# Kernel optimization log

Measured on AMD Instinct MI355X. Metric: run time of the kernel, lower is better.

The kernel has to match this reference:

```python
import jax, jax.numpy as jnp
import numpy as np

N, E, D, D_OUT = 100000, 3200000, 64, 64
EPS = 1e-5


def setup_inputs() -> dict:
    key = jax.random.key(0)
    ks = jax.random.split(key, 16)
    s = 1.0 / np.sqrt(D)
    inp = {
        "x": jax.random.normal(ks[0], (N, D), dtype=jnp.float32),
        "edge_index": jax.random.randint(ks[1], (2, E), 0, N, dtype=jnp.int64),
        # layer 1: GCNConv weight/bias, fc weight/bias, BN gamma/beta
        "W1": jax.random.uniform(ks[2], (D, D), jnp.float32, -s, s),
        "b1": jnp.zeros((D,), jnp.float32),
        "fw1": jax.random.uniform(ks[3], (D, D), jnp.float32, -s, s),
        "fb1": jax.random.uniform(ks[4], (D,), jnp.float32, -s, s),
        "g1": jnp.ones((D,), jnp.float32),
        "bt1": jnp.zeros((D,), jnp.float32),
        # layer 2
        "W2": jax.random.uniform(ks[5], (D, D), jnp.float32, -s, s),
        "b2": jnp.zeros((D,), jnp.float32),
        "fw2": jax.random.uniform(ks[6], (D, D_OUT), jnp.float32, -s, s),
        "fb2": jax.random.uniform(ks[7], (D_OUT,), jnp.float32, -s, s),
        "g2": jnp.ones((D_OUT,), jnp.float32),
        "bt2": jnp.zeros((D_OUT,), jnp.float32),
    }
    return inp


def _gcn_conv(x, W, b, src, dst, dinv):
    # x' = X W, then symmetric-normalized scatter-add aggregation (self loops included)
    h = x @ W                                   # [N, D]
    msg = (dinv[src] * dinv[dst])[:, None] * h[src]  # [E+N, D]
    out = jax.ops.segment_sum(msg, dst, num_segments=N)
    return out + b


def _fc_bn_relu(x, fw, fb, g, bt):
    y = x @ fw + fb
    mu = jnp.mean(y, axis=0)
    var = jnp.mean((y - mu) ** 2, axis=0)  # biased var (torch BN training mode)
    y = (y - mu) * jax.lax.rsqrt(var + EPS) * g + bt
    return jax.nn.relu(y)


def reference(x, edge_index, W1, b1, fw1, fb1, g1, bt1, W2, b2, fw2, fb2, g2, bt2):
    loop = jnp.arange(N, dtype=edge_index.dtype)
    src = jnp.concatenate([edge_index[0], loop])  # add self loops
    dst = jnp.concatenate([edge_index[1], loop])
    deg = jax.ops.segment_sum(jnp.ones_like(dst, dtype=x.dtype), dst, num_segments=N)
    dinv = jax.lax.rsqrt(deg)  # deg >= 1 thanks to self loops

    h = _gcn_conv(x, W1, b1, src, dst, dinv)
    h = _fc_bn_relu(h, fw1, fb1, g1, bt1)
    h = _gcn_conv(h, W2, b2, src, dst, dinv)
    h = _fc_bn_relu(h, fw2, fb2, g2, bt2)
    return h
```

## Files before the change

### kernel.cpp

```cpp
#include <hip/hip_runtime.h>

#define N_NODES 100000
#define N_EDGES 3200000
#define D 64
#define EPS 1e-5f

#define BSHIFT 7
#define BNODES 128
#define NBUCK ((N_NODES + BNODES - 1) / BNODES)
#define P1_CHUNK 4096
#define NB_P1 ((N_EDGES + P1_CHUNK - 1) / P1_CHUNK)
#define SRC_MASK 0x1FFFFu
#define BCAP 4480
#define TBL_STRIDE 784

typedef _Float16 f16x8 __attribute__((ext_vector_type(8)));
typedef _Float16 half2v __attribute__((ext_vector_type(2)));
typedef unsigned int u32x4 __attribute__((ext_vector_type(4)));
typedef __attribute__((ext_vector_type(4))) float f32x4;

__device__ __forceinline__ unsigned short f2h(float f) {
  return __builtin_bit_cast(unsigned short, (_Float16)f);
}
__device__ __forceinline__ half2v u2h(unsigned int u) {
  return __builtin_bit_cast(half2v, u);
}
__device__ __forceinline__ unsigned int h2u(half2v h) {
  return __builtin_bit_cast(unsigned int, h);
}
__device__ __forceinline__ float2 hpair(unsigned int u) {
  half2v h = __builtin_bit_cast(half2v, u);
  return make_float2((float)h.x, (float)h.y);
}
__device__ __forceinline__ void addp(half2v a[4], uint4 u) {
  a[0] += u2h(u.x);
  a[1] += u2h(u.y);
  a[2] += u2h(u.z);
  a[3] += u2h(u.w);
}

__global__ __launch_bounds__(256) void combine_weights(
    const float* __restrict__ W1, const float* __restrict__ b1,
    const float* __restrict__ fw1, const float* __restrict__ fb1,
    const float* __restrict__ W2, const float* __restrict__ b2,
    const float* __restrict__ fw2, const float* __restrict__ fb2,
    unsigned int* __restrict__ WcB1, float* __restrict__ bc1,
    unsigned int* __restrict__ WcB2, float* __restrict__ bc2,
    float* __restrict__ stats) {
  if (blockIdx.x == 2) {
    if (threadIdx.x < 256) stats[threadIdx.x] = 0.0f;
    return;
  }
  const float* W  = blockIdx.x ? W2  : W1;
  const float* fw = blockIdx.x ? fw2 : fw1;
  const float* b  = blockIdx.x ? b2  : b1;
  const float* fb = blockIdx.x ? fb2 : fb1;
  unsigned int* WcB = blockIdx.x ? WcB2 : WcB1;
  float* bc = blockIdx.x ? bc2 : bc1;

  __shared__ float sW[64 * 64];
  __shared__ float sf[64 * 64];
  __shared__ float sC[64 * 64];
  for (int i = threadIdx.x; i < 4096; i += 256) { sW[i] = W[i]; sf[i] = fw[i]; }
  __syncthreads();
  for (int o = threadIdx.x; o < 4096; o += 256) {
    int i = o >> 6, j = o & 63;
    float acc = 0.f;
    #pragma unroll
    for (int k = 0; k < 64; ++k) acc += sW[i * 64 + k] * sf[k * 64 + j];
    sC[o] = acc;
  }
  __syncthreads();
  for (int o = threadIdx.x; o < 2048; o += 256) {
    int jj = o & 3, L = (o >> 2) & 63, kh = (o >> 8) & 1, nt = o >> 9;
    int k0 = (L >> 4) * 8 + jj * 2 + kh * 32;
    int n  = nt * 16 + (L & 15);
    unsigned int lo = f2h(sC[k0 * 64 + n]);
    unsigned int hi = f2h(sC[(k0 + 1) * 64 + n]);
    WcB[o] = (hi << 16) | lo;
  }
  if (threadIdx.x < 64) {
    int j = threadIdx.x;
    float acc = fb[j];
    #pragma unroll
    for (int k = 0; k < 64; ++k) acc += b[k] * sf[k * 64 + j];
    bc[j] = acc;
  }
}

__global__ __launch_bounds__(256) void pass1_sort(
    const int* __restrict__ src, const int* __restrict__ dst,
    unsigned int* __restrict__ stage, unsigned short* __restrict__ tbl) {
  __shared__ unsigned int hist[NBUCK];
  __shared__ unsigned int ts[256];
  __shared__ unsigned int sorted[P1_CHUNK];
  const int tid = threadIdx.x;
  const int e0 = blockIdx.x * P1_CHUNK;

  for (int b = tid; b < NBUCK; b += 256) hist[b] = 0;
  __syncthreads();

  int dreg[16];
  #pragma unroll
  for (int k = 0; k < 16; ++k) {
    int e = e0 + k * 256 + tid;
    int d = (e < N_EDGES) ? dst[e] : -1;
    dreg[k] = d;
    if (d >= 0) atomicAdd(&hist[((unsigned)d) >> BSHIFT], 1u);
  }
  __syncthreads();

  unsigned int v[4], run = 0;
  #pragma unroll
  for (int j = 0; j < 4; ++j) {
    int bk = 4 * tid + j;
    unsigned int h = (bk < NBUCK) ? hist[bk] : 0u;
    v[j] = run;
    run += h;
  }
  ts[tid] = run;
  __syncthreads();
  for (int o = 1; o < 256; o <<= 1) {
    unsigned int add = (tid >= o) ? ts[tid - o] : 0u;
    __syncthreads();
    ts[tid] += add;
    __syncthreads();
  }
  const unsigned int excl = ts[tid] - run;
  const unsigned int m = ts[255];
  unsigned short* trow = tbl + (size_t)blockIdx.x * TBL_STRIDE;
  #pragma unroll
  for (int j = 0; j < 4; ++j) {
    int bk = 4 * tid + j;
    if (bk < NBUCK) {
      unsigned int o = excl + v[j];
      hist[bk] = o;
      trow[bk] = (unsigned short)o;
    }
  }
  if (tid == 0) trow[NBUCK] = (unsigned short)m;
  __syncthreads();

  #pragma unroll
  for (int k = 0; k < 16; ++k) {
    int e = e0 + k * 256 + tid;
    int t = dreg[k];
    if (t >= 0) {
      unsigned int pos = atomicAdd(&hist[((unsigned)t) >> BSHIFT], 1u);
      sorted[pos] = (((unsigned)(t & (BNODES - 1))) << 17) | (unsigned)src[e];
    }
  }
  __syncthreads();

  unsigned int* so = stage + (size_t)blockIdx.x * P1_CHUNK;
  for (int i = tid; i < (int)m; i += 256) so[i] = sorted[i];
}

__global__ __launch_bounds__(512) void pass2_sort(
    const unsigned int* __restrict__ stage, const unsigned short* __restrict__ tbl,
    int* __restrict__ eSrc, int* __restrict__ off, int* __restrict__ edeg,
    float* __restrict__ dinv, const float* __restrict__ x,
    unsigned short* __restrict__ Xs) {
  __shared__ int spre[512];
  __shared__ int cnt[BNODES];
  __shared__ int ts[BNODES];
  __shared__ float dinvL[BNODES];
  __shared__ unsigned int raw[BCAP];
  __shared__ int sorted[BCAP];
  const int b = blockIdx.x, tid = threadIdx.x;
  const int n0 = b * BNODES;

  int base0 = 0, base1 = 0, len0 = 0, len1 = 0;
  {
    int s0 = 2 * tid, s1 = 2 * tid + 1;
    if (s0 < NB_P1) {
      const unsigned short* trow = tbl + (size_t)s0 * TBL_STRIDE;
      int o0 = trow[b], o1 = trow[b + 1];
      base0 = s0 * P1_CHUNK + o0;
      len0 = o1 - o0;
    }
    if (s1 < NB_P1) {
      const unsigned short* trow = tbl + (size_t)s1 * TBL_STRIDE;
      int o0 = trow[b], o1 = trow[b + 1];
      base1 = s1 * P1_CHUNK + o0;
      len1 = o1 - o0;
    }
  }
  if (tid < BNODES) cnt[tid] = 0;
  const int mylen = len0 + len1;
  spre[tid] = mylen;
  __syncthreads();
  for (int o = 1; o < 512; o <<= 1) {
    int add = (tid >= o) ? spre[tid - o] : 0;
    __syncthreads();
    spre[tid] += add;
    __syncthreads();
  }
  const int m = spre[511];
  const int pref = spre[tid] - mylen;

  for (int j = 0; j < len0; ++j) {
    unsigned int p = stage[base0 + j];
    raw[pref + j] = p;
    atomicAdd(&cnt[p >> 17], 1);
  }
  for (int j = 0; j < len1; ++j) {
    unsigned int p = stage[base1 + j];
    raw[pref + len0 + j] = p;
    atomicAdd(&cnt[p >> 17], 1);
  }
  __syncthreads();

  int v = 0;
  if (tid < BNODES) { v = cnt[tid]; ts[tid] = v; }
  __syncthreads();
  for (int o = 1; o < BNODES; o <<= 1) {
    int add = (tid >= o && tid < BNODES) ? ts[tid - o] : 0;
    __syncthreads();
    if (tid < BNODES) ts[tid] += add;
    __syncthreads();
  }
  if (tid < BNODES) {
    int excl = ts[tid] - v;
    int node = n0 + tid;
    float dv = rsqrtf((float)v + 1.0f);
    dinvL[tid] = dv;
    if (node < N_NODES) {
      off[node]  = b * BCAP + excl;
      edeg[node] = v;
      dinv[node] = dv;
    }
    cnt[tid] = excl;
  }
  __syncthreads();

  for (int i = tid; i < m; i += 512) {
    unsigned int p = raw[i];
    int pos = atomicAdd(&cnt[p >> 17], 1);
    if (pos < BCAP) sorted[pos] = (int)(p & SRC_MASK);
  }
  __syncthreads();

  int* out = eSrc + (size_t)b * BCAP;
  for (int i = tid; i < m; i += 512) out[i] = sorted[i];

  const int rows = min(BNODES, N_NODES - n0);
  for (int i = tid; i < rows * 64; i += 512) {
    int r = i >> 6;
    size_t g = (size_t)(n0 + r) * 64 + (i & 63);
    Xs[g] = f2h(dinvL[r] * x[g]);
  }
}

__global__ __launch_bounds__(256) void agg_csr(
    const int* __restrict__ off, const int* __restrict__ edeg,
    const int* __restrict__ eSrc, const unsigned short* __restrict__ Xs,
    const float* __restrict__ dinv, unsigned short* __restrict__ agg) {
  const int wv = (blockIdx.x * 256 + threadIdx.x) >> 6;
  const int lane = threadIdx.x & 63;
  const int half = lane >> 5;
  const int l32 = lane & 31;
  const int grp = l32 >> 3;
  const int sub = lane & 7;
  const int node = wv * 2 + half;
  if (node >= N_NODES) return;

  const int s0 = off[node];
  const int deg = edeg[node];
  const float dvf = dinv[node];
  const uint4* XsV = (const uint4*)Xs;

  int eidx = node;
  if (deg > 0) {
    int li = (l32 < deg) ? l32 : deg - 1;
    eidx = __builtin_nontemporal_load(&eSrc[s0 + li]);
  }

  half2v acc[4];
  {
    uint4 u = XsV[(size_t)node * 8 + sub];
    if (l32 >= 8) { u.x = 0; u.y = 0; u.z = 0; u.w = 0; }
    acc[0] = u2h(u.x);
    acc[1] = u2h(u.y);
    acc[2] = u2h(u.z);
    acc[3] = u2h(u.w);
  }

  uint4 g[8];
  #pragma unroll
  for (int j = 0; j < 8; ++j) {
    int srcn = __shfl(eidx, half * 32 + j * 4 + grp, 64);
    g[j] = XsV[(size_t)srcn * 8 + sub];
  }
  #pragma unroll
  for (int j = 0; j < 8; ++j) {
    uint4 u = g[j];
    if (j * 4 + grp >= deg) { u.x = 0; u.y = 0; u.z = 0; u.w = 0; }
    addp(acc, u);
  }

  if (deg > 32) {
    const int lim = deg - 1;
    for (int e = 32; e < deg; e += 4) {
      int ee = e + grp;
      int srcn = __builtin_nontemporal_load(&eSrc[s0 + min(ee, lim)]);
      uint4 u = XsV[(size_t)srcn * 8 + sub];
      if (ee > lim) { u.x = 0; u.y = 0; u.z = 0; u.w = 0; }
      addp(acc, u);
    }
  }

  #pragma unroll
  for (int mk = 8; mk <= 16; mk <<= 1) {
    #pragma unroll
    for (int i = 0; i < 4; ++i)
      acc[i] += u2h(__shfl_xor(h2u(acc[i]), mk, 64));
  }

  if (l32 < 8) {
    _Float16 dh = (_Float16)dvf;
    half2v d2 = {dh, dh};
    u32x4 o;
    o.x = h2u(acc[0] * d2);
    o.y = h2u(acc[1] * d2);
    o.z = h2u(acc[2] * d2);
    o.w = h2u(acc[3] * d2);
    __builtin_nontemporal_store(o, (u32x4*)(agg + (size_t)node * 64 + sub * 8));
  }
}

__global__ __launch_bounds__(256) void gemm_stats(
    const unsigned short* __restrict__ A, const unsigned int* __restrict__ WcB,
    const float* __restrict__ bc, unsigned short* __restrict__ Yb,
    float* __restrict__ colsum, float* __restrict__ colsq) {
  const int tid = threadIdx.x;
  const int L = tid & 63, wv = tid >> 6;
  const int quad = L >> 4, l16 = L & 15;

  const f16x8* Wv = (const f16x8*)WcB;
  f16x8 bfr[4][2];
  #pragma unroll
  for (int nt = 0; nt < 4; ++nt)
    #pragma unroll
    for (int kh = 0; kh < 2; ++kh)
      bfr[nt][kh] = Wv[(nt * 2 + kh) * 64 + L];
  float bcv[4];
  #pragma unroll
  for (int nt = 0; nt < 4; ++nt) bcv[nt] = bc[nt * 16 + l16];

  const f16x8* Av = (const f16x8*)A;
  float psum[4] = {0.f, 0.f, 0.f, 0.f}, psq[4] = {0.f, 0.f, 0.f, 0.f};

  #pragma unroll
  for (int loop = 0; loop < 2; ++loop) {
    const int rowbase = blockIdx.x * 128 + loop * 64 + wv * 16;
    const int m = min(rowbase + l16, N_NODES - 1);
    f16x8 a0 = Av[(size_t)m * 8 + quad];
    f16x8 a1 = Av[(size_t)m * 8 + 4 + quad];
    #pragma unroll
    for (int nt = 0; nt < 4; ++nt) {
      f32x4 acc = {0.f, 0.f, 0.f, 0.f};
      acc = __builtin_amdgcn_mfma_f32_16x16x32_f16(a0, bfr[nt][0], acc, 0, 0, 0);
      acc = __builtin_amdgcn_mfma_f32_16x16x32_f16(a1, bfr[nt][1], acc, 0, 0, 0);
      #pragma unroll
      for (int r = 0; r < 4; ++r) {
        int row = rowbase + quad * 4 + r;
        if (row < N_NODES) {
          float y = acc[r] + bcv[nt];
          Yb[(size_t)row * 64 + nt * 16 + l16] = f2h(y);
          psum[nt] += y;
          psq[nt] += y * y;
        }
      }
    }
  }

  #pragma unroll
  for (int nt = 0; nt < 4; ++nt) {
    psum[nt] += __shfl_xor(psum[nt], 16, 64);
    psum[nt] += __shfl_xor(psum[nt], 32, 64);
    psq[nt]  += __shfl_xor(psq[nt], 16, 64);
    psq[nt]  += __shfl_xor(psq[nt], 32, 64);
  }
  __shared__ float rsum[4][64];
  __shared__ float rsq[4][64];
  if (L < 16) {
    #pragma unroll
    for (int nt = 0; nt < 4; ++nt) {
      rsum[wv][nt * 16 + L] = psum[nt];
      rsq[wv][nt * 16 + L]  = psq[nt];
    }
  }
  __syncthreads();
  if (tid < 64) {
    float s = rsum[0][tid] + rsum[1][tid] + rsum[2][tid] + rsum[3][tid];
    float q = rsq[0][tid] + rsq[1][tid] + rsq[2][tid] + rsq[3][tid];
    atomicAdd(&colsum[tid], s);
    atomicAdd(&colsq[tid], q);
  }
}

__global__ __launch_bounds__(256) void prescale_y(
    unsigned short* __restrict__ YbXs, const float* __restrict__ dinv,
    const float* __restrict__ colsum, const float* __restrict__ colsq,
    const float* __restrict__ g, const float* __restrict__ bt) {
  __shared__ float sa[64], sc[64];
  if (threadIdx.x < 64) {
    int j = threadIdx.x;
    float mu = colsum[j] * (1.0f / N_NODES);
    float var = colsq[j] * (1.0f / N_NODES) - mu * mu;
    float s = rsqrtf(var + EPS) * g[j];
    sa[j] = s;
    sc[j] = bt[j] - mu * s;
  }
  __syncthreads();
  int idx = blockIdx.x * blockDim.x + threadIdx.x;
  if (idx < N_NODES * 8) {
    int r = idx >> 3, c0 = (idx & 7) * 8;
    float dv = dinv[r];
    uint4 u = ((const uint4*)YbXs)[idx];
    float2 p0 = hpair(u.x), p1 = hpair(u.y), p2 = hpair(u.z), p3 = hpair(u.w);
    p0.x = dv * fmaxf(fmaf(p0.x, sa[c0    ], sc[c0    ]), 0.f);
    p0.y = dv * fmaxf(fmaf(p0.y, sa[c0 + 1], sc[c0 + 1]), 0.f);
    p1.x = dv * fmaxf(fmaf(p1.x, sa[c0 + 2], sc[c0 + 2]), 0.f);
    p1.y = dv * fmaxf(fmaf(p1.y, sa[c0 + 3], sc[c0 + 3]), 0.f);
    p2.x = dv * fmaxf(fmaf(p2.x, sa[c0 + 4], sc[c0 + 4]), 0.f);
    p2.y = dv * fmaxf(fmaf(p2.y, sa[c0 + 5], sc[c0 + 5]), 0.f);
    p3.x = dv * fmaxf(fmaf(p3.x, sa[c0 + 6], sc[c0 + 6]), 0.f);
    p3.y = dv * fmaxf(fmaf(p3.y, sa[c0 + 7], sc[c0 + 7]), 0.f);
    uint4 o;
    o.x = ((unsigned)f2h(p0.y) << 16) | f2h(p0.x);
    o.y = ((unsigned)f2h(p1.y) << 16) | f2h(p1.x);
    o.z = ((unsigned)f2h(p2.y) << 16) | f2h(p2.x);
    o.w = ((unsigned)f2h(p3.y) << 16) | f2h(p3.x);
    ((uint4*)YbXs)[idx] = o;
  }
}

__global__ __launch_bounds__(256) void final_norm(
    const unsigned short* __restrict__ Yb, float* __restrict__ out,
    const float* __restrict__ colsum, const float* __restrict__ colsq,
    const float* __restrict__ g, const float* __restrict__ bt) {
  __shared__ float sa[64], sc[64];
  if (threadIdx.x < 64) {
    int j = threadIdx.x;
    float mu = colsum[j] * (1.0f / N_NODES);
    float var = colsq[j] * (1.0f / N_NODES) - mu * mu;
    float s = rsqrtf(var + EPS) * g[j];
    sa[j] = s;
    sc[j] = bt[j] - mu * s;
  }
  __syncthreads();
  int idx = blockIdx.x * blockDim.x + threadIdx.x;
  if (idx < N_NODES * 8) {
    int c0 = (idx & 7) * 8;
    uint4 u = ((const uint4*)Yb)[idx];
    float2 p0 = hpair(u.x), p1 = hpair(u.y), p2 = hpair(u.z), p3 = hpair(u.w);
    float4 o0, o1;
    o0.x = fmaxf(fmaf(p0.x, sa[c0    ], sc[c0    ]), 0.f);
    o0.y = fmaxf(fmaf(p0.y, sa[c0 + 1], sc[c0 + 1]), 0.f);
    o0.z = fmaxf(fmaf(p1.x, sa[c0 + 2], sc[c0 + 2]), 0.f);
    o0.w = fmaxf(fmaf(p1.y, sa[c0 + 3], sc[c0 + 3]), 0.f);
    o1.x = fmaxf(fmaf(p2.x, sa[c0 + 4], sc[c0 + 4]), 0.f);
    o1.y = fmaxf(fmaf(p2.y, sa[c0 + 5], sc[c0 + 5]), 0.f);
    o1.z = fmaxf(fmaf(p3.x, sa[c0 + 6], sc[c0 + 6]), 0.f);
    o1.w = fmaxf(fmaf(p3.y, sa[c0 + 7], sc[c0 + 7]), 0.f);
    ((float4*)out)[idx * 2] = o0;
    ((float4*)out)[idx * 2 + 1] = o1;
  }
}

extern "C" void kernel_launch(void* const* d_in, const int* in_sizes, int n_in,
                              void* d_out, int out_size, void* d_ws, size_t ws_size,
                              hipStream_t stream) {
  const float* x   = (const float*)d_in[0];
  const int*   src = (const int*)d_in[1];
  const int*   dst = src + N_EDGES;
  const float* W1  = (const float*)d_in[2];
  const float* b1  = (const float*)d_in[3];
  const float* fw1 = (const float*)d_in[4];
  const float* fb1 = (const float*)d_in[5];
  const float* g1  = (const float*)d_in[6];
  const float* bt1 = (const float*)d_in[7];
  const float* W2  = (const float*)d_in[8];
  const float* b2  = (const float*)d_in[9];
  const float* fw2 = (const float*)d_in[10];
  const float* fb2 = (const float*)d_in[11];
  const float* g2  = (const float*)d_in[12];
  const float* bt2 = (const float*)d_in[13];

  float* out = (float*)d_out;

  unsigned char* w = (unsigned char*)d_ws;
  unsigned int*   stage = (unsigned int*)w;
  unsigned short* aggb  = (unsigned short*)w;
  size_t ofs = ((size_t)NB_P1 * P1_CHUNK * 4 + 255) & ~(size_t)255;
  float*          dinv  = (float*)(w + ofs);
  unsigned short* XsYb  = (unsigned short*)(dinv + N_NODES);
  int*            eSrc  = (int*)(XsYb + (size_t)N_NODES * D);
  int*            off   = eSrc + (size_t)NBUCK * BCAP;
  int*            edeg  = off + N_NODES;
  unsigned short* tbl   = (unsigned short*)(edeg + N_NODES);
  unsigned int* WcB1 = (unsigned int*)(tbl + (size_t)NB_P1 * TBL_STRIDE);
  float* bc1  = (float*)(WcB1 + 2048);
  unsigned int* WcB2 = (unsigned int*)(bc1 + 64);
  float* bc2  = (float*)(WcB2 + 2048);
  float* sum1 = bc2 + 64;
  float* sq1  = sum1 + 64;
  float* sum2 = sq1 + 64;
  float* sq2  = sum2 + 64;

  const int nv = N_NODES * 8;
  const int nagg = (N_NODES + 7) / 8;
  dim3 blk(256);

  combine_weights<<<3, blk, 0, stream>>>(W1, b1, fw1, fb1, W2, b2, fw2, fb2,
                                         WcB1, bc1, WcB2, bc2, sum1);
  pass1_sort<<<NB_P1, blk, 0, stream>>>(src, dst, stage, tbl);
  pass2_sort<<<NBUCK, 512, 0, stream>>>(stage, tbl, eSrc, off, edeg, dinv, x, XsYb);
  agg_csr<<<nagg, blk, 0, stream>>>(off, edeg, eSrc, XsYb, dinv, aggb);
  gemm_stats<<<(N_NODES + 127) / 128, blk, 0, stream>>>(aggb, WcB1, bc1, XsYb, sum1, sq1);
  prescale_y<<<(nv + 255) / 256, blk, 0, stream>>>(XsYb, dinv, sum1, sq1, g1, bt1);
  agg_csr<<<nagg, blk, 0, stream>>>(off, edeg, eSrc, XsYb, dinv, aggb);
  gemm_stats<<<(N_NODES + 127) / 128, blk, 0, stream>>>(aggb, WcB2, bc2, XsYb, sum2, sq2);
  final_norm<<<(nv + 255) / 256, blk, 0, stream>>>(XsYb, out, sum2, sq2, g2, bt2);
}
```

Measured before the change: 328.0 us.

## Fuse CSR aggregation with MFMA GEMM and column statistics via shared memory

Merges the gather-aggregation kernel and the GEMM+stats kernel into one 512-thread block. Each block aggregates 32 nodes into LDS, then runs the MFMA product with the combined weights on those rows. This removes the fp16 aggregate round trip through global memory and one launch per layer. Y now goes to a separate workspace buffer, so prescale reads Y and writes Xs out of place. The cost is more column-stat atomics (one block per 32 rows instead of 128), more LDS per block, and a block-wide barrier between the gather and GEMM phases.

```diff
diff --git a/kernel.cpp b/kernel.cpp
--- a/kernel.cpp
+++ b/kernel.cpp
@@ -252,156 +252,131 @@
   }
 }
 
-__global__ __launch_bounds__(256) void agg_csr(
+__global__ __launch_bounds__(512) void agg_gemm(
     const int* __restrict__ off, const int* __restrict__ edeg,
     const int* __restrict__ eSrc, const unsigned short* __restrict__ Xs,
-    const float* __restrict__ dinv, unsigned short* __restrict__ agg) {
-  const int wv = (blockIdx.x * 256 + threadIdx.x) >> 6;
-  const int lane = threadIdx.x & 63;
-  const int half = lane >> 5;
-  const int l32 = lane & 31;
-  const int grp = l32 >> 3;
-  const int sub = lane & 7;
-  const int node = wv * 2 + half;
-  if (node >= N_NODES) return;
-
-  const int s0 = off[node];
-  const int deg = edeg[node];
-  const float dvf = dinv[node];
-  const uint4* XsV = (const uint4*)Xs;
-
-  int eidx = node;
-  if (deg > 0) {
-    int li = (l32 < deg) ? l32 : deg - 1;
-    eidx = __builtin_nontemporal_load(&eSrc[s0 + li]);
-  }
-
-  half2v acc[4];
-  {
-    uint4 u = XsV[(size_t)node * 8 + sub];
-    if (l32 >= 8) { u.x = 0; u.y = 0; u.z = 0; u.w = 0; }
-    acc[0] = u2h(u.x);
-    acc[1] = u2h(u.y);
-    acc[2] = u2h(u.z);
-    acc[3] = u2h(u.w);
-  }
-
-  uint4 g[8];
-  #pragma unroll
-  for (int j = 0; j < 8; ++j) {
-    int srcn = __shfl(eidx, half * 32 + j * 4 + grp, 64);
-    g[j] = XsV[(size_t)srcn * 8 + sub];
-  }
-  #pragma unroll
-  for (int j = 0; j < 8; ++j) {
-    uint4 u = g[j];
-    if (j * 4 + grp >= deg) { u.x = 0; u.y = 0; u.z = 0; u.w = 0; }
-    addp(acc, u);
-  }
-
-  if (deg > 32) {
-    const int lim = deg - 1;
-    for (int e = 32; e < deg; e += 4) {
-      int ee = e + grp;
-      int srcn = __builtin_nontemporal_load(&eSrc[s0 + min(ee, lim)]);
-      uint4 u = XsV[(size_t)srcn * 8 + sub];
-      if (ee > lim) { u.x = 0; u.y = 0; u.z = 0; u.w = 0; }
-      addp(acc, u);
-    }
-  }
-
-  #pragma unroll
-  for (int mk = 8; mk <= 16; mk <<= 1) {
-    #pragma unroll
-    for (int i = 0; i < 4; ++i)
-      acc[i] += u2h(__shfl_xor(h2u(acc[i]), mk, 64));
-  }
-
-  if (l32 < 8) {
-    _Float16 dh = (_Float16)dvf;
-    half2v d2 = {dh, dh};
-    u32x4 o;
-    o.x = h2u(acc[0] * d2);
-    o.y = h2u(acc[1] * d2);
-    o.z = h2u(acc[2] * d2);
-    o.w = h2u(acc[3] * d2);
-    __builtin_nontemporal_store(o, (u32x4*)(agg + (size_t)node * 64 + sub * 8));
-  }
-}
-
-__global__ __launch_bounds__(256) void gemm_stats(
-    const unsigned short* __restrict__ A, const unsigned int* __restrict__ WcB,
+    const float* __restrict__ dinv, const unsigned int* __restrict__ WcB,
     const float* __restrict__ bc, unsigned short* __restrict__ Yb,
     float* __restrict__ colsum, float* __restrict__ colsq) {
+  __shared__ __align__(16) unsigned int sY[32 * 36];
+  __shared__ float rsum[2][64];
+  __shared__ float rsq[2][64];
   const int tid = threadIdx.x;
-  const int L = tid & 63, wv = tid >> 6;
-  const int quad = L >> 4, l16 = L & 15;
-
+  const int wv = tid >> 6;
+  const int lane = tid & 63;
+  const int half = lane >> 5, l32 = lane & 31;
+  const int grp = l32 >> 3, sub = lane & 7;
+  const int quad = lane >> 4, l16 = lane & 15;
+  const uint4* XsV = (const uint4*)Xs;
+
+  const int nt = wv >> 1, rb = wv & 1;
   const f16x8* Wv = (const f16x8*)WcB;
-  f16x8 bfr[4][2];
+  const f16x8 bfr0 = Wv[(nt * 2 + 0) * 64 + lane];
+  const f16x8 bfr1 = Wv[(nt * 2 + 1) * 64 + lane];
+  const float bcv = bc[nt * 16 + l16];
+
   #pragma unroll
-  for (int nt = 0; nt < 4; ++nt)
+  for (int p = 0; p < 2; ++p) {
+    const int node = blockIdx.x * 32 + p * 16 + wv * 2 + half;
+    const int s0 = off[node];
+    const int deg = edeg[node];
+    const float dvf = dinv[node];
+
+    int eidx = node;
+    if (deg > 0) {
+      int li = (l32 < deg) ? l32 : deg - 1;
+      eidx = __builtin_nontemporal_load(&eSrc[s0 + li]);
+    }
+
+    half2v acc[4];
+    {
+      uint4 u = XsV[(size_t)node * 8 + sub];
+      if (l32 >= 8) { u.x = 0; u.y = 0; u.z = 0; u.w = 0; }
+      acc[0] = u2h(u.x);
+      acc[1] = u2h(u.y);
+      acc[2] = u2h(u.z);
+      acc[3] = u2h(u.w);
+    }
+
+    uint4 g[8];
     #pragma unroll
-    for (int kh = 0; kh < 2; ++kh)
-      bfr[nt][kh] = Wv[(nt * 2 + kh) * 64 + L];
-  float bcv[4];
-  #pragma unroll
-  for (int nt = 0; nt < 4; ++nt) bcv[nt] = bc[nt * 16 + l16];
-
-  const f16x8* Av = (const f16x8*)A;
-  float psum[4] = {0.f, 0.f, 0.f, 0.f}, psq[4] = {0.f, 0.f, 0.f, 0.f};
-
-  #pragma unroll
-  for (int loop = 0; loop < 2; ++loop) {
-    const int rowbase = blockIdx.x * 128 + loop * 64 + wv * 16;
-    const int m = min(rowbase + l16, N_NODES - 1);
-    f16x8 a0 = Av[(size_t)m * 8 + quad];
-    f16x8 a1 = Av[(size_t)m * 8 + 4 + quad];
+    for (int j = 0; j < 8; ++j) {
+      int srcn = __shfl(eidx, half * 32 + j * 4 + grp, 64);
+      g[j] = XsV[(size_t)srcn * 8 + sub];
+    }
     #pragma unroll
-    for (int nt = 0; nt < 4; ++nt) {
-      f32x4 acc = {0.f, 0.f, 0.f, 0.f};
-      acc = __builtin_amdgcn_mfma_f32_16x16x32_f16(a0, bfr[nt][0], acc, 0, 0, 0);
-      acc = __builtin_amdgcn_mfma_f32_16x16x32_f16(a1, bfr[nt][1], acc, 0, 0, 0);
+    for (int j = 0; j < 8; ++j) {
+      uint4 u = g[j];
+      if (j * 4 + grp >= deg) { u.x = 0; u.y = 0; u.z = 0; u.w = 0; }
+      addp(acc, u);
+    }
+    if (deg > 32) {
+      const int lim = deg - 1;
+      for (int e = 32; e < deg; e += 4) {
+        int ee = e + grp;
+        int srcn = __builtin_nontemporal_load(&eSrc[s0 + min(ee, lim)]);
+        uint4 u = XsV[(size_t)srcn * 8 + sub];
+        if (ee > lim) { u.x = 0; u.y = 0; u.z = 0; u.w = 0; }
+        addp(acc, u);
+      }
+    }
+
+    #pragma unroll
+    for (int mk = 8; mk <= 16; mk <<= 1) {
       #pragma unroll
-      for (int r = 0; r < 4; ++r) {
-        int row = rowbase + quad * 4 + r;
-        if (row < N_NODES) {
-          float y = acc[r] + bcv[nt];
-          Yb[(size_t)row * 64 + nt * 16 + l16] = f2h(y);
-          psum[nt] += y;
-          psq[nt] += y * y;
-        }
-      }
-    }
-  }
-
-  #pragma unroll
-  for (int nt = 0; nt < 4; ++nt) {
-    psum[nt] += __shfl_xor(psum[nt], 16, 64);
-    psum[nt] += __shfl_xor(psum[nt], 32, 64);
-    psq[nt]  += __shfl_xor(psq[nt], 16, 64);
-    psq[nt]  += __shfl_xor(psq[nt], 32, 64);
-  }
-  __shared__ float rsum[4][64];
-  __shared__ float rsq[4][64];
-  if (L < 16) {
+      for (int i = 0; i < 4; ++i)
+        acc[i] += u2h(__shfl_xor(h2u(acc[i]), mk, 64));
+    }
+
+    if (l32 < 8) {
+      _Float16 dh = (_Float16)dvf;
+      half2v d2 = {dh, dh};
+      u32x4 o;
+      o.x = h2u(acc[0] * d2);
+      o.y = h2u(acc[1] * d2);
+      o.z = h2u(acc[2] * d2);
+      o.w = h2u(acc[3] * d2);
+      int row = p * 16 + wv * 2 + half;
+      *(u32x4*)&sY[row * 36 + sub * 4] = o;
+    }
+  }
+  __syncthreads();
+
+  {
+    const int rowbase = blockIdx.x * 32 + rb * 16;
+    f16x8 a0 = *(const f16x8*)&sY[(rb * 16 + l16) * 36 + quad * 4];
+    f16x8 a1 = *(const f16x8*)&sY[(rb * 16 + l16) * 36 + (4 + quad) * 4];
+    f32x4 acc = {0.f, 0.f, 0.f, 0.f};
+    acc = __builtin_amdgcn_mfma_f32_16x16x32_f16(a0, bfr0, acc, 0, 0, 0);
+    acc = __builtin_amdgcn_mfma_f32_16x16x32_f16(a1, bfr1, acc, 0, 0, 0);
+    float psum = 0.f, psq = 0.f;
     #pragma unroll
-    for (int nt = 0; nt < 4; ++nt) {
-      rsum[wv][nt * 16 + L] = psum[nt];
-      rsq[wv][nt * 16 + L]  = psq[nt];
+    for (int r = 0; r < 4; ++r) {
+      int row = rowbase + quad * 4 + r;
+      float y = acc[r] + bcv;
+      Yb[(size_t)row * 64 + nt * 16 + l16] = f2h(y);
+      psum += y;
+      psq += y * y;
+    }
+    psum += __shfl_xor(psum, 16, 64);
+    psum += __shfl_xor(psum, 32, 64);
+    psq  += __shfl_xor(psq, 16, 64);
+    psq  += __shfl_xor(psq, 32, 64);
+    if (lane < 16) {
+      rsum[rb][nt * 16 + lane] = psum;
+      rsq[rb][nt * 16 + lane]  = psq;
     }
   }
   __syncthreads();
   if (tid < 64) {
-    float s = rsum[0][tid] + rsum[1][tid] + rsum[2][tid] + rsum[3][tid];
-    float q = rsq[0][tid] + rsq[1][tid] + rsq[2][tid] + rsq[3][tid];
-    atomicAdd(&colsum[tid], s);
-    atomicAdd(&colsq[tid], q);
+    atomicAdd(&colsum[tid], rsum[0][tid] + rsum[1][tid]);
+    atomicAdd(&colsq[tid],  rsq[0][tid] + rsq[1][tid]);
   }
 }
 
 __global__ __launch_bounds__(256) void prescale_y(
-    unsigned short* __restrict__ YbXs, const float* __restrict__ dinv,
+    const unsigned short* __restrict__ Yin, unsigned short* __restrict__ Xout,
+    const float* __restrict__ dinv,
     const float* __restrict__ colsum, const float* __restrict__ colsq,
     const float* __restrict__ g, const float* __restrict__ bt) {
   __shared__ float sa[64], sc[64];
@@ -418,7 +393,7 @@
   if (idx < N_NODES * 8) {
     int r = idx >> 3, c0 = (idx & 7) * 8;
     float dv = dinv[r];
-    uint4 u = ((const uint4*)YbXs)[idx];
+    uint4 u = ((const uint4*)Yin)[idx];
     float2 p0 = hpair(u.x), p1 = hpair(u.y), p2 = hpair(u.z), p3 = hpair(u.w);
     p0.x = dv * fmaxf(fmaf(p0.x, sa[c0    ], sc[c0    ]), 0.f);
     p0.y = dv * fmaxf(fmaf(p0.y, sa[c0 + 1], sc[c0 + 1]), 0.f);
@@ -433,7 +408,7 @@
     o.y = ((unsigned)f2h(p1.y) << 16) | f2h(p1.x);
     o.z = ((unsigned)f2h(p2.y) << 16) | f2h(p2.x);
     o.w = ((unsigned)f2h(p3.y) << 16) | f2h(p3.x);
-    ((uint4*)YbXs)[idx] = o;
+    ((uint4*)Xout)[idx] = o;
   }
 }
 
@@ -493,7 +468,7 @@
 
   unsigned char* w = (unsigned char*)d_ws;
   unsigned int*   stage = (unsigned int*)w;
-  unsigned short* aggb  = (unsigned short*)w;
+  unsigned short* Ybuf  = (unsigned short*)w;
   size_t ofs = ((size_t)NB_P1 * P1_CHUNK * 4 + 255) & ~(size_t)255;
   float*          dinv  = (float*)(w + ofs);
   unsigned short* XsYb  = (unsigned short*)(dinv + N_NODES);
@@ -511,17 +486,16 @@
   float* sq2  = sum2 + 64;
 
   const int nv = N_NODES * 8;
-  const int nagg = (N_NODES + 7) / 8;
   dim3 blk(256);
 
   combine_weights<<<3, blk, 0, stream>>>(W1, b1, fw1, fb1, W2, b2, fw2, fb2,
                                          WcB1, bc1, WcB2, bc2, sum1);
   pass1_sort<<<NB_P1, blk, 0, stream>>>(src, dst, stage, tbl);
   pass2_sort<<<NBUCK, 512, 0, stream>>>(stage, tbl, eSrc, off, edeg, dinv, x, XsYb);
-  agg_csr<<<nagg, blk, 0, stream>>>(off, edeg, eSrc, XsYb, dinv, aggb);
-  gemm_stats<<<(N_NODES + 127) / 128, blk, 0, stream>>>(aggb, WcB1, bc1, XsYb, sum1, sq1);
-  prescale_y<<<(nv + 255) / 256, blk, 0, stream>>>(XsYb, dinv, sum1, sq1, g1, bt1);
-  agg_csr<<<nagg, blk, 0, stream>>>(off, edeg, eSrc, XsYb, dinv, aggb);
-  gemm_stats<<<(N_NODES + 127) / 128, blk, 0, stream>>>(aggb, WcB2, bc2, XsYb, sum2, sq2);
-  final_norm<<<(nv + 255) / 256, blk, 0, stream>>>(XsYb, out, sum2, sq2, g2, bt2);
-}
+  agg_gemm<<<N_NODES / 32, 512, 0, stream>>>(off, edeg, eSrc, XsYb, dinv,
+                                             WcB1, bc1, Ybuf, sum1, sq1);
+  prescale_y<<<(nv + 255) / 256, blk, 0, stream>>>(Ybuf, XsYb, dinv, sum1, sq1, g1, bt1);
+  agg_gemm<<<N_NODES / 32, 512, 0, stream>>>(off, edeg, eSrc, XsYb, dinv,
+                                             WcB2, bc2, Ybuf, sum2, sq2);
+  final_norm<<<(nv + 255) / 256, blk, 0, stream>>>(Ybuf, out, sum2, sq2, g2, bt2);
+}
```

Result: slower. 373.2 us (+13.8%).
